# Kernel tuning notes

Hardware: AMD Instinct MI355X
Metric: run time of the kernel (lower is better)

Reference implementation:

```python
import jax, jax.numpy as jnp
import numpy as np

DIM = 2048
KV_DIM = 1024
NUM_HEADS = 16
HEAD_DIM = DIM // NUM_HEADS  # 128
EPS = 1e-6
B, LQ, LKV = 2, 4096, 1024


def _rope_cos_sin(L, d, base=10000.0):
    inv_freq = 1.0 / (base ** (np.arange(0, d, 2, dtype=np.float32) / d))  # [d/2]
    freqs = np.arange(L, dtype=np.float32)[:, None] * inv_freq[None, :]   # [L, d/2]
    emb = np.concatenate([freqs, freqs], axis=-1)                          # [L, d]
    return jnp.asarray(np.cos(emb)), jnp.asarray(np.sin(emb))


def setup_inputs() -> dict:
    key = jax.random.key(0)
    ks = jax.random.split(key, 10)
    x = jax.random.normal(ks[0], (B, LQ, DIM), dtype=jnp.float32)
    y = jax.random.normal(ks[1], (B, LKV, KV_DIM), dtype=jnp.float32)
    xc, xs = _rope_cos_sin(LQ, HEAD_DIM)
    yc, ys = _rope_cos_sin(LKV, HEAD_DIM)
    x_cos = jnp.broadcast_to(xc[None], (B, LQ, HEAD_DIM))
    x_sin = jnp.broadcast_to(xs[None], (B, LQ, HEAD_DIM))
    y_cos = jnp.broadcast_to(yc[None], (B, LKV, HEAD_DIM))
    y_sin = jnp.broadcast_to(ys[None], (B, LKV, HEAD_DIM))
    s = 0.02
    Wq = jax.random.normal(ks[2], (DIM, DIM), dtype=jnp.float32) * s
    Wk = jax.random.normal(ks[3], (DIM, KV_DIM), dtype=jnp.float32) * s
    Wv = jax.random.normal(ks[4], (DIM, KV_DIM), dtype=jnp.float32) * s
    Wo = jax.random.normal(ks[5], (DIM, DIM), dtype=jnp.float32) * s
    bq = jnp.zeros((DIM,), jnp.float32)
    bk = jnp.zeros((DIM,), jnp.float32)
    bv = jnp.zeros((DIM,), jnp.float32)
    bo = jnp.zeros((DIM,), jnp.float32)
    rmsq_w = jnp.ones((DIM,), jnp.float32)
    rmsk_w = jnp.ones((DIM,), jnp.float32)
    ln_w = jnp.ones((KV_DIM,), jnp.float32)
    ln_b = jnp.zeros((KV_DIM,), jnp.float32)
    return dict(x=x, y=y, x_cos=x_cos, x_sin=x_sin, y_cos=y_cos, y_sin=y_sin,
                Wq=Wq, bq=bq, Wk=Wk, bk=bk, Wv=Wv, bv=bv, Wo=Wo, bo=bo,
                rmsq_w=rmsq_w, rmsk_w=rmsk_w, ln_w=ln_w, ln_b=ln_b)


def _rms_norm(t, w, eps=EPS):
    return t * jax.lax.rsqrt(jnp.mean(t * t, axis=-1, keepdims=True) + eps) * w


def _layer_norm(t, w, b, eps=EPS):
    mu = jnp.mean(t, axis=-1, keepdims=True)
    var = jnp.mean(jnp.square(t - mu), axis=-1, keepdims=True)
    return (t - mu) * jax.lax.rsqrt(var + eps) * w + b


def _rotate_half(t):
    d2 = t.shape[-1] // 2
    return jnp.concatenate([-t[..., d2:], t[..., :d2]], axis=-1)


def _apply_rope(t, cos, sin):
    # t: [B, L, H, D]; cos/sin: [B, L, D] -> unsqueeze head dim (unsqueeze_dim=2)
    cos = cos[:, :, None, :]
    sin = sin[:, :, None, :]
    return t * cos + _rotate_half(t) * sin


def _block_forward(x, y, x_cos, x_sin, y_cos, y_sin,
                   Wq, bq, Wk, bk, Wv, bv, Wo, bo,
                   rmsq_w, rmsk_w, ln_w, ln_b):
    Bb, Lq, D = x.shape
    Lk = y.shape[1]
    H, Dh = NUM_HEADS, HEAD_DIM
    # y pre-norm (block-level LayerNorm)
    yn = _layer_norm(y, ln_w, ln_b)
    # projections + RMSNorm on q/k
    q = _rms_norm(x @ Wq.T + bq, rmsq_w)   # [B, Lq, D]
    k = _rms_norm(yn @ Wk.T + bk, rmsk_w)  # [B, Lk, D]
    v = yn @ Wv.T + bv                     # [B, Lk, D]
    # split heads and apply RoPE
    q = _apply_rope(q.reshape(Bb, Lq, H, Dh), x_cos, x_sin)
    k = _apply_rope(k.reshape(Bb, Lk, H, Dh), y_cos, y_sin)
    v = v.reshape(Bb, Lk, H, Dh)
    # non-causal cross attention, scale = 1/sqrt(head_dim)
    scale = 1.0 / jnp.sqrt(jnp.asarray(Dh, q.dtype))
    scores = jnp.einsum('blhd,bmhd->bhlm', q, k) * scale
    probs = jax.nn.softmax(scores, axis=-1)
    out = jnp.einsum('bhlm,bmhd->blhd', probs, v).reshape(Bb, Lq, D)
    return out @ Wo.T + bo


def reference(x, y, x_cos, x_sin, y_cos, y_sin,
              Wq, bq, Wk, bk, Wv, bv, Wo, bo,
              rmsq_w, rmsk_w, ln_w, ln_b):
    return _block_forward(x, y, x_cos, x_sin, y_cos, y_sin,
                          Wq, bq, Wk, bk, Wv, bv, Wo, bo,
                          rmsq_w, rmsk_w, ln_w, ln_b)
```

## Files before the change

kernel.cpp:

```cpp
#include <hip/hip_runtime.h>


typedef __attribute__((ext_vector_type(8))) short    short8;
typedef __attribute__((ext_vector_type(8))) unsigned short ushort8;
typedef __attribute__((ext_vector_type(4))) unsigned short ushort4v;
typedef __attribute__((ext_vector_type(4))) float    f32x4;
typedef __attribute__((ext_vector_type(16))) float   f32x16;
typedef __attribute__((ext_vector_type(4))) unsigned int uint4v;

#define DEV __device__ __forceinline__

DEV unsigned short f2bf(float f) {
  unsigned int u = __builtin_bit_cast(unsigned int, f);
  u += 0x7FFFu + ((u >> 16) & 1u);
  return (unsigned short)(u >> 16);
}
DEV float bf2f(unsigned short h) {
  return __builtin_bit_cast(float, ((unsigned int)h) << 16);
}
DEV unsigned int cvtpk_bf16(float lo, float hi) {
  unsigned int r;
  asm("v_cvt_pk_bf16_f32 %0, %1, %2" : "=v"(r) : "v"(lo), "v"(hi));
  return r;
}
DEV short8 mk8(unsigned a, unsigned b, unsigned c, unsigned d) {
  uint4v t; t.x = a; t.y = b; t.z = c; t.w = d;
  return __builtin_bit_cast(short8, t);
}

DEV void gload_lds16(const void* g, void* l) {
  __builtin_amdgcn_global_load_lds(
      (const __attribute__((address_space(1))) void*)g,
      (__attribute__((address_space(3))) void*)l, 16, 0, 0);
}

__global__ __launch_bounds__(256) void prep_kernel(const float* __restrict__ y,
                                                   const float* __restrict__ lnw,
                                                   const float* __restrict__ lnb,
                                                   unsigned short* __restrict__ yn,
                                                   const float* __restrict__ x,
                                                   const float* __restrict__ Wq,
                                                   const float* __restrict__ Wk,
                                                   const float* __restrict__ Wv,
                                                   const float* __restrict__ Wo,
                                                   unsigned short* __restrict__ xb,
                                                   unsigned short* __restrict__ Wqb,
                                                   unsigned short* __restrict__ Wkb,
                                                   unsigned short* __restrict__ Wvb,
                                                   unsigned short* __restrict__ Wob) {
  const int t = threadIdx.x;
  if (blockIdx.x < 2048) {
    const int row = blockIdx.x;
    const float* yr = y + (size_t)row * 1024;
    float4 v = *(const float4*)(yr + t * 4);
    float s1 = v.x + v.y + v.z + v.w;
    float s2 = v.x * v.x + v.y * v.y + v.z * v.z + v.w * v.w;
#pragma unroll
    for (int m = 1; m < 64; m <<= 1) {
      s1 += __shfl_xor(s1, m);
      s2 += __shfl_xor(s2, m);
    }
    __shared__ float red[8];
    const int wave = t >> 6, lane = t & 63;
    if (lane == 0) { red[wave] = s1; red[4 + wave] = s2; }
    __syncthreads();
    s1 = red[0] + red[1] + red[2] + red[3];
    s2 = red[4] + red[5] + red[6] + red[7];
    const float mu = s1 * (1.0f / 1024.0f);
    const float var = s2 * (1.0f / 1024.0f) - mu * mu;
    const float rs = rsqrtf(var + 1e-6f);
    ushort4v o;
    o.x = f2bf((v.x - mu) * rs * lnw[t * 4 + 0] + lnb[t * 4 + 0]);
    o.y = f2bf((v.y - mu) * rs * lnw[t * 4 + 1] + lnb[t * 4 + 1]);
    o.z = f2bf((v.z - mu) * rs * lnw[t * 4 + 2] + lnb[t * 4 + 2]);
    o.w = f2bf((v.w - mu) * rs * lnw[t * 4 + 3] + lnb[t * 4 + 3]);
    *(ushort4v*)(yn + (size_t)row * 1024 + t * 4) = o;
    return;
  }
  const int nx = 4194304, nwq = 1048576, nwk = 524288, nwv = 524288;
  const int total = 7340032;
  int i = (blockIdx.x - 2048) * 256 + t;
  const int stride = 1536 * 256;
  for (; i < total; i += stride) {
    int j = i;
    const float* s; unsigned short* d;
    if (j < nx) { s = x; d = xb; }
    else if ((j -= nx) < nwq) { s = Wq; d = Wqb; }
    else if ((j -= nwq) < nwk) { s = Wk; d = Wkb; }
    else if ((j -= nwk) < nwv) { s = Wv; d = Wvb; }
    else { j -= nwv; s = Wo; d = Wob; }
    float4 v = *(const float4*)(s + (size_t)j * 4);
    ushort4v o;
    o.x = f2bf(v.x); o.y = f2bf(v.y); o.z = f2bf(v.z); o.w = f2bf(v.w);
    *(ushort4v*)(d + (size_t)j * 4) = o;
  }
}

template <int EPI>
DEV void gemm256_body(const unsigned short* __restrict__ A,
                      const unsigned short* __restrict__ W,
                      const float* __restrict__ bias0,
                      const float* __restrict__ bias1,
                      int nsplit, void* __restrict__ Cout,
                      int M, int N, int K, int ldRow,
                      int bidLocal, int nwg, char* ldsb, int tid) {
  const int wave = tid >> 6, lane = tid & 63;
  const int lg = lane >> 4, l15 = lane & 15;
  const int wm = wave >> 2, wn = wave & 3;

  const int wgid = (bidLocal & 7) * (nwg >> 3) + (bidLocal >> 3);
  const int nbn = N >> 8;
  const int m0 = (wgid / nbn) * 256;
  const int n0 = (wgid % nbn) * 256;

  const char* Ab = (const char*)A;
  const char* Wb = (const char*)W;
  const size_t ld = (size_t)ldRow * 2;
  const int NT = K >> 6;
  const int NI = NT >> 1;

  const int prow = tid >> 3;
  const int psw  = ((tid * 16) & 127) ^ ((prow & 7) << 4);
  const int pdst = tid * 16;
  const char* pAg = Ab + (size_t)(m0 + prow) * ld + psw;
  const char* pBg = Wb + (size_t)(n0 + prow) * ld + psw;

  f32x4 acc[8][4] = {};
  short8 af[4][2];
  short8 bf[4][2];

#define LDSB(BUF, SEG) (ldsb + ((BUF) * 4 + (SEG)) * 16384)

#define STG(BUF, HALF, ISB, TAU) do {                                         \
    const char* _g = ((ISB) ? pBg : pAg) + (size_t)(HALF) * 128 * ld +        \
                     (size_t)(TAU) * 128;                                     \
    char* _l = LDSB(BUF, (ISB) * 2 + (HALF));                                 \
    gload_lds16(_g, _l + pdst);                                               \
    gload_lds16(_g + 64 * ld, _l + pdst + 8192);                              \
  } while (0)

#define LDA(BUF, H) do {                                                      \
    const char* _b = LDSB(BUF, wm);                                           \
    _Pragma("unroll") for (int mfl = 0; mfl < 4; ++mfl) {                     \
      const int _r = (H) * 64 + mfl * 16 + l15;                               \
      _Pragma("unroll") for (int ks = 0; ks < 2; ++ks)                        \
        af[mfl][ks] = *(const short8*)(_b + _r * 128 +                        \
                        ((ks * 64 + lg * 16) ^ ((_r & 7) << 4)));             \
    }                                                                         \
  } while (0)

#define LDB(BUF, G) do {                                                      \
    const char* _b = LDSB(BUF, 2 + (wn >> 1));                                \
    _Pragma("unroll") for (int nfl = 0; nfl < 2; ++nfl) {                     \
      const int _r = (wn & 1) * 64 + (G) * 32 + nfl * 16 + l15;               \
      _Pragma("unroll") for (int ks = 0; ks < 2; ++ks)                        \
        bf[(G) * 2 + nfl][ks] = *(const short8*)(_b + _r * 128 +              \
                        ((ks * 64 + lg * 16) ^ ((_r & 7) << 4)));             \
    }                                                                         \
  } while (0)

#define MFMA_Q(H, G) do {                                                     \
    __builtin_amdgcn_s_setprio(1);                                            \
    _Pragma("unroll") for (int ks = 0; ks < 2; ++ks)                          \
    _Pragma("unroll") for (int mfl = 0; mfl < 4; ++mfl)                       \
    _Pragma("unroll") for (int nfl = 0; nfl < 2; ++nfl)                       \
      acc[(H) * 4 + mfl][(G) * 2 + nfl] =                                     \
        __builtin_amdgcn_mfma_f32_16x16x32_bf16(af[mfl][ks],                  \
            bf[(G) * 2 + nfl][ks], acc[(H) * 4 + mfl][(G) * 2 + nfl], 0,0,0); \
    __builtin_amdgcn_s_setprio(0);                                            \
  } while (0)

#define BAR() __builtin_amdgcn_s_barrier()
#define VM4() asm volatile("s_waitcnt vmcnt(4)" ::: "memory")
#define VM0() asm volatile("s_waitcnt vmcnt(0)" ::: "memory")

  STG(0, 0, 0, 0); STG(0, 1, 0, 0); STG(0, 0, 1, 0); STG(0, 1, 1, 0);
  STG(1, 0, 1, 1); STG(1, 1, 1, 1);
  VM4(); BAR();

  for (int t = 0; t < NI - 1; ++t) {
    const int t2 = 2 * t;
    LDA(0, 0); LDB(0, 0); STG(1, 0, 0, t2 + 1);
    BAR(); MFMA_Q(0, 0); BAR();
    LDB(0, 1); STG(1, 1, 0, t2 + 1);
    BAR(); MFMA_Q(0, 1); BAR();
    LDA(0, 1); STG(0, 0, 1, t2 + 2);
    BAR(); MFMA_Q(1, 1); BAR();
    STG(0, 1, 1, t2 + 2);
    BAR(); MFMA_Q(1, 0); VM4(); BAR();
    LDA(1, 0); LDB(1, 0); STG(0, 0, 0, t2 + 2);
    BAR(); MFMA_Q(0, 0); BAR();
    LDB(1, 1); STG(0, 1, 0, t2 + 2);
    BAR(); MFMA_Q(0, 1); BAR();
    LDA(1, 1); STG(1, 0, 1, t2 + 3);
    BAR(); MFMA_Q(1, 1); BAR();
    STG(1, 1, 1, t2 + 3);
    BAR(); MFMA_Q(1, 0); VM4(); BAR();
  }

  LDA(0, 0); LDB(0, 0); STG(1, 0, 0, NT - 1);
  BAR(); MFMA_Q(0, 0); BAR();
  LDB(0, 1); STG(1, 1, 0, NT - 1);
  BAR(); MFMA_Q(0, 1); BAR();
  LDA(0, 1);
  BAR(); MFMA_Q(1, 1); BAR();
  BAR(); MFMA_Q(1, 0); VM0(); BAR();
  LDA(1, 0); LDB(1, 0); MFMA_Q(0, 0);
  LDB(1, 1); MFMA_Q(0, 1);
  LDA(1, 1); MFMA_Q(1, 1);
  MFMA_Q(1, 0);

#undef STG
#undef LDA
#undef LDB
#undef MFMA_Q
#undef BAR
#undef VM4
#undef VM0
#undef LDSB

#pragma unroll
  for (int nf = 0; nf < 4; ++nf) {
    const int n = n0 + wn * 64 + nf * 16 + l15;
    float bv = 0.f;
    if constexpr (EPI != 2) bv = (n < nsplit) ? bias0[n] : bias1[n - nsplit];
#pragma unroll
    for (int mf = 0; mf < 8; ++mf) {
      const int mB = m0 + wm * 128 + mf * 16 + lg * 4;
#pragma unroll
      for (int r = 0; r < 4; ++r) {
        const float v = acc[mf][nf][r] + bv;
        if constexpr (EPI == 1)
          ((float*)Cout)[(size_t)(mB + r) * N + n] = v;
        else
          ((unsigned short*)Cout)[(size_t)(mB + r) * N + n] = f2bf(v);
      }
    }
  }
}

__global__ __launch_bounds__(512, 2) void gemm_dual(const unsigned short* __restrict__ xb,
                                                    const unsigned short* __restrict__ Wqb,
                                                    const float* __restrict__ bq,
                                                    unsigned short* __restrict__ qpre,
                                                    const unsigned short* __restrict__ ynb,
                                                    const unsigned short* __restrict__ Wkb,
                                                    unsigned short* __restrict__ kvpA,
                                                    unsigned short* __restrict__ kvpB) {
  __shared__ __align__(16) char lds[2][4][16384];
  gemm256_body<0>(xb, Wqb, bq, bq, 2048, qpre, 8192, 2048, 2048, 2048,
                  blockIdx.x, 256, &lds[0][0][0], threadIdx.x);
  __syncthreads();
  const int kvt = blockIdx.x & 127, khalf = blockIdx.x >> 7;
  gemm256_body<2>(ynb + khalf * 512, Wkb + khalf * 512, nullptr, nullptr, 0,
                  khalf ? kvpB : kvpA, 2048, 4096, 512, 1024,
                  kvt, 128, &lds[0][0][0], threadIdx.x);
}

__global__ __launch_bounds__(512, 2) void gemm_f32(const unsigned short* __restrict__ A,
                                                   const unsigned short* __restrict__ W,
                                                   const float* __restrict__ bias,
                                                   float* __restrict__ C,
                                                   int M, int N, int K) {
  __shared__ __align__(16) char lds[2][4][16384];
  gemm256_body<1>(A, W, bias, bias, N, C, M, N, K, K,
                  blockIdx.x, 256, &lds[0][0][0], threadIdx.x);
}

DEV void rmsrope2_body(const unsigned short* __restrict__ in,
                       const unsigned short* __restrict__ in2,
                       const float* __restrict__ bias,
                       const float* __restrict__ w,
                       const float* __restrict__ cs,
                       const float* __restrict__ sn,
                       unsigned short* __restrict__ out,
                       int L, int ldin, float scale, int row,
                       float* srow, float* red) {
  const int t = threadIdx.x;
  ushort8 v = *(const ushort8*)(in + (size_t)row * ldin + t * 8);
  float vals[8];
  if (in2) {
    ushort8 v2 = *(const ushort8*)(in2 + (size_t)row * ldin + t * 8);
#pragma unroll
    for (int j = 0; j < 8; ++j) vals[j] = bf2f(v[j]) + bf2f(v2[j]) + bias[t * 8 + j];
  } else {
#pragma unroll
    for (int j = 0; j < 8; ++j) vals[j] = bf2f(v[j]);
  }
  float ss = 0.f;
#pragma unroll
  for (int j = 0; j < 8; ++j) { ss += vals[j] * vals[j]; srow[t * 8 + j] = vals[j]; }
#pragma unroll
  for (int m = 1; m < 64; m <<= 1) ss += __shfl_xor(ss, m);
  const int wave = t >> 6, lane = t & 63;
  if (lane == 0) red[wave] = ss;
  __syncthreads();
  const float tot = red[0] + red[1] + red[2] + red[3];
  const float rms = rsqrtf(tot * (1.0f / 2048.0f) + 1e-6f);

  const int n0 = t * 8;
  const int d0 = n0 & 127;
  const int hh = n0 >> 7;
  const float sign = (d0 < 64) ? -1.0f : 1.0f;
  const float* cb = cs + (size_t)row * 128 + d0;
  const float* sb = sn + (size_t)row * 128 + d0;
  ushort8 ou;
#pragma unroll
  for (int j = 0; j < 8; ++j) {
    const float self = vals[j] * rms * w[n0 + j];
    const float part = srow[(n0 ^ 64) + j] * rms * w[(n0 ^ 64) + j];
    ou[j] = f2bf((self * cb[j] + sign * part * sb[j]) * scale);
  }
  const int b = row / L, l = row - (row / L) * L;
  *(ushort8*)(out + (((size_t)(b * 16 + hh)) * L + l) * 128 + d0) = ou;
}

DEV void vtrans2_body(const unsigned short* __restrict__ va,
                      const unsigned short* __restrict__ vb,
                      const float* __restrict__ bv,
                      unsigned short* __restrict__ vt, int ldv, int bid,
                      unsigned short (*lt)[130]) {
  const int kt = bid & 15, bh = bid >> 4;
  const int h = bh & 15, b = bh >> 4;
  const int t = threadIdx.x;
  const int i0 = t >> 4, c0 = (t & 15) * 8;
  const size_t sbase = ((size_t)(b * 1024 + kt * 64)) * ldv + h * 128;
#pragma unroll
  for (int ii = 0; ii < 4; ++ii) {
    const int i = i0 + ii * 16;
    ushort8 a = *(const ushort8*)(va + sbase + (size_t)i * ldv + c0);
    ushort8 bb = *(const ushort8*)(vb + sbase + (size_t)i * ldv + c0);
#pragma unroll
    for (int j = 0; j < 8; ++j)
      lt[i][c0 + j] = f2bf(bf2f(a[j]) + bf2f(bb[j]) + bv[h * 128 + c0 + j]);
  }
  __syncthreads();
  const int d0 = t >> 3, j0 = (t & 7) * 8;
  unsigned short* dst = vt + (size_t)bh * 128 * 1024 + kt * 64;
#pragma unroll
  for (int dd = 0; dd < 4; ++dd) {
    const int d = d0 + dd * 32;
    ushort8 o;
#pragma unroll
    for (int jj = 0; jj < 8; ++jj) o[jj] = lt[j0 + jj][d];
    *(ushort8*)(dst + (size_t)d * 1024 + j0) = o;
  }
}

__global__ __launch_bounds__(256) void post_kernel(const unsigned short* __restrict__ qpre,
                                                   const float* __restrict__ rmsq_w,
                                                   const float* __restrict__ x_cos,
                                                   const float* __restrict__ x_sin,
                                                   unsigned short* __restrict__ qr,
                                                   const unsigned short* __restrict__ kvpA,
                                                   const unsigned short* __restrict__ kvpB,
                                                   const float* __restrict__ bk,
                                                   const float* __restrict__ bv,
                                                   const float* __restrict__ rmsk_w,
                                                   const float* __restrict__ y_cos,
                                                   const float* __restrict__ y_sin,
                                                   unsigned short* __restrict__ kr,
                                                   unsigned short* __restrict__ vt,
                                                   float qscale) {
  __shared__ __align__(16) float srow[2048];
  __shared__ float red[4];
  __shared__ unsigned short lt[64][130];
  const int b = blockIdx.x;
  if (b < 8192) {
    rmsrope2_body(qpre, nullptr, nullptr, rmsq_w, x_cos, x_sin, qr,
                  4096, 2048, qscale, b, srow, red);
  } else if (b < 10240) {
    rmsrope2_body(kvpA, kvpB, bk, rmsk_w, y_cos, y_sin, kr,
                  1024, 4096, 1.0f, b - 8192, srow, red);
  } else {
    vtrans2_body(kvpA + 2048, kvpB + 2048, bv, vt, 4096, b - 10240, lt);
  }
}

__global__ __launch_bounds__(256, 2) void attn_kernel(const unsigned short* __restrict__ q,
                                                      const unsigned short* __restrict__ k,
                                                      const unsigned short* __restrict__ vt,
                                                      unsigned short* __restrict__ ao) {
  __shared__ __align__(16) char sK[2][64 * 256];
  __shared__ __align__(16) char sV[2][64 * 256];

  const int bid0 = blockIdx.x;
  const int bid = (bid0 & 7) * 128 + (bid0 >> 3);
  const int qt = bid & 31, bh = bid >> 5;
  const int tid = threadIdx.x;
  const int wave = tid >> 6, lane = tid & 63;
  const int l31 = lane & 31, hi = lane >> 5;
  const bool hib = (hi != 0);

  const unsigned short* qbase = q + (((size_t)bh * 4096) + qt * 128 + wave * 32) * 128;
  const char* kbase = (const char*)(k + (size_t)bh * 1024 * 128);
  const char* vbase = (const char*)(vt + (size_t)bh * 128 * 1024);

  short8 qb[8];
#pragma unroll
  for (int step = 0; step < 8; ++step)
    qb[step] = *(const short8*)(qbase + (size_t)l31 * 128 + step * 16 + hi * 8);

  f32x16 o[4] = {};
  float lsum = 0.f;

#define STAGE_KV(BUF, KV0) do {                                              \
    _Pragma("unroll")                                                        \
    for (int i = 0; i < 4; ++i) {                                            \
      const int p = (i * 256 + tid) * 16;                                    \
      const int row = p >> 8;                                                \
      const int si = (p & 255) ^ ((row & 15) << 4);                          \
      gload_lds16(kbase + (size_t)((KV0) + row) * 256 + si, sK[BUF] + p);    \
    }                                                                        \
    _Pragma("unroll")                                                        \
    for (int i = 0; i < 4; ++i) {                                            \
      const int p = (i * 256 + tid) * 16;                                    \
      const int row = p >> 8;                                                \
      const int si = (p & 255) ^ ((row & 15) << 4);                          \
      const int d = 2 * row + (si >> 7);                                     \
      gload_lds16(vbase + (size_t)d * 2048 + (KV0) * 2 + (si & 127),         \
                  sV[BUF] + p);                                              \
    }                                                                        \
  } while (0)

#define QK(K, S0, S1) do {                                                   \
    const int ksw = (l31 & 15) << 4;                                         \
    _Pragma("unroll") for (int step = 0; step < 8; ++step) {                 \
      const int cb2 = step * 32 + hi * 16;                                   \
      short8 kf0 = *(const short8*)((K) + l31 * 256 + (cb2 ^ ksw));          \
      short8 kf1 = *(const short8*)((K) + (32 + l31) * 256 + (cb2 ^ ksw));   \
      S0 = __builtin_amdgcn_mfma_f32_32x32x16_bf16(kf0, qb[step], S0, 0,0,0);\
      S1 = __builtin_amdgcn_mfma_f32_32x32x16_bf16(kf1, qb[step], S1, 0,0,0);\
    }                                                                        \
  } while (0)

#define SOFTMAX_PV(V, SS, F) do {                                            \
    float p_[16];                                                            \
    _Pragma("unroll") for (int r = 0; r < 16; ++r) p_[r] = exp2f((SS)[r]);   \
    lsum += (((p_[0]+p_[1])+(p_[2]+p_[3])) + ((p_[4]+p_[5])+(p_[6]+p_[7])))  \
          + (((p_[8]+p_[9])+(p_[10]+p_[11])) + ((p_[12]+p_[13])+(p_[14]+p_[15])));\
    const unsigned w0 = cvtpk_bf16(p_[0], p_[1]),  w1 = cvtpk_bf16(p_[2], p_[3]), \
                   w2 = cvtpk_bf16(p_[4], p_[5]),  w3 = cvtpk_bf16(p_[6], p_[7]), \
                   w4 = cvtpk_bf16(p_[8], p_[9]),  w5 = cvtpk_bf16(p_[10], p_[11]),\
                   w6 = cvtpk_bf16(p_[12], p_[13]),w7 = cvtpk_bf16(p_[14], p_[15]);\
    const unsigned x0 = (unsigned)__shfl_xor((int)(hib ? w0 : w2), 32);      \
    const unsigned x1 = (unsigned)__shfl_xor((int)(hib ? w1 : w3), 32);      \
    const unsigned x2 = (unsigned)__shfl_xor((int)(hib ? w4 : w6), 32);      \
    const unsigned x3 = (unsigned)__shfl_xor((int)(hib ? w5 : w7), 32);      \
    const short8 fr0 = mk8(hib ? x0 : w0, hib ? x1 : w1,                     \
                           hib ? w2 : x0, hib ? w3 : x1);                    \
    const short8 fr1 = mk8(hib ? x2 : w4, hib ? x3 : w5,                     \
                           hib ? w6 : x2, hib ? w7 : x3);                    \
    _Pragma("unroll") for (int kstep = 0; kstep < 2; ++kstep) {              \
      const short8 pa = kstep ? fr1 : fr0;                                   \
      const int colb = (F) * 64 + kstep * 32 + hi * 16;                      \
      _Pragma("unroll") for (int dt = 0; dt < 4; ++dt) {                     \
        const int vrow = dt * 16 + (l31 >> 1);                               \
        const int inner = (l31 & 1) * 128 + colb;                            \
        short8 vf = *(const short8*)((V) + vrow * 256 +                      \
                                     (inner ^ ((vrow & 15) << 4)));          \
        o[dt] = __builtin_amdgcn_mfma_f32_32x32x16_bf16(pa, vf, o[dt], 0,0,0);\
      }                                                                      \
    }                                                                        \
  } while (0)

#define TILE(BUF) do {                                                       \
    f32x16 s0 = {}, s1 = {};                                                 \
    QK(sK[BUF], s0, s1);                                                     \
    SOFTMAX_PV(sV[BUF], s0, 0);                                              \
    SOFTMAX_PV(sV[BUF], s1, 1);                                              \
  } while (0)

  STAGE_KV(0, 0);
  __syncthreads();

#pragma unroll 1
  for (int kt2 = 0; kt2 < 8; ++kt2) {
    STAGE_KV(1, (2 * kt2 + 1) * 64);
    TILE(0);
    __syncthreads();
    if (kt2 < 7) STAGE_KV(0, (2 * kt2 + 2) * 64);
    TILE(1);
    __syncthreads();
  }
#undef STAGE_KV
#undef QK
#undef SOFTMAX_PV
#undef TILE

  lsum += __shfl_xor(lsum, 32);
  const float linv = 1.0f / lsum;
  const int b = bh >> 4, h = bh & 15;
#pragma unroll
  for (int r = 0; r < 16; ++r) {
    const int crow = (r & 3) + 8 * (r >> 2) + 4 * hi;
    const float inv = __shfl(linv, crow);
    const int qg = qt * 128 + wave * 32 + crow;
    const size_t orow = ((size_t)b * 4096 + qg) * 2048 + h * 128;
#pragma unroll
    for (int dt = 0; dt < 4; ++dt)
      ao[orow + dt * 32 + l31] = f2bf(o[dt][r] * inv);
  }
}

extern "C" void kernel_launch(void* const* d_in, const int* in_sizes, int n_in,
                              void* d_out, int out_size, void* d_ws, size_t ws_size,
                              hipStream_t stream) {
  (void)in_sizes; (void)n_in; (void)out_size; (void)ws_size;
  const float* x      = (const float*)d_in[0];
  const float* y      = (const float*)d_in[1];
  const float* x_cos  = (const float*)d_in[2];
  const float* x_sin  = (const float*)d_in[3];
  const float* y_cos  = (const float*)d_in[4];
  const float* y_sin  = (const float*)d_in[5];
  const float* Wq     = (const float*)d_in[6];
  const float* bq     = (const float*)d_in[7];
  const float* Wk     = (const float*)d_in[8];
  const float* bk     = (const float*)d_in[9];
  const float* Wv     = (const float*)d_in[10];
  const float* bv     = (const float*)d_in[11];
  const float* Wo     = (const float*)d_in[12];
  const float* bo     = (const float*)d_in[13];
  const float* rmsq_w = (const float*)d_in[14];
  const float* rmsk_w = (const float*)d_in[15];
  const float* ln_w   = (const float*)d_in[16];
  const float* ln_b   = (const float*)d_in[17];

  char* ws = (char*)d_ws;
  unsigned short* xb    = (unsigned short*)(ws + 0);
  unsigned short* Wqb   = (unsigned short*)(ws + 33554432);
  unsigned short* Wkb   = (unsigned short*)(ws + 41943040);
  unsigned short* Wvb   = (unsigned short*)(ws + 46137344);
  unsigned short* Wob   = (unsigned short*)(ws + 50331648);
  unsigned short* ynb   = (unsigned short*)(ws + 58720256);
  unsigned short* qpre  = (unsigned short*)(ws + 62914560);
  unsigned short* kvpA  = (unsigned short*)(ws + 96468992);
  unsigned short* kvpB  = (unsigned short*)(ws + 113246208);
  unsigned short* qr    = xb;
  unsigned short* kr    = Wqb;
  unsigned short* vt    = Wkb;
  unsigned short* ao    = qpre;
  (void)Wvb;

  const float qscale = 1.4426950408889634f * 0.08838834764831843f;

  prep_kernel<<<3584, 256, 0, stream>>>(y, ln_w, ln_b, ynb, x, Wq, Wk, Wv, Wo,
                                        xb, Wqb, Wkb, Wvb, Wob);
  gemm_dual<<<256, 512, 0, stream>>>(xb, Wqb, bq, qpre, ynb, Wkb, kvpA, kvpB);
  post_kernel<<<10752, 256, 0, stream>>>(qpre, rmsq_w, x_cos, x_sin, qr,
                                         kvpA, kvpB, bk, bv, rmsk_w,
                                         y_cos, y_sin, kr, vt, qscale);
  attn_kernel<<<1024, 256, 0, stream>>>(qr, kr, vt, ao);
  gemm_f32<<<256, 512, 0, stream>>>(ao, Wob, bo, (float*)d_out, 8192, 2048, 2048);
}
```

Before: 302.7 us.

## Switch projection GEMM to 32x32x16 bf16 MFMA with paired-row LDS swizzle

Replaces the 16x16x32 MFMA tiling in the shared 256x256 GEMM body with 32x32x16 MFMA. The LDS layout becomes two rows per 256-byte line with a 16-way XOR swizzle, and the fragment loads and epilogue row mapping are rewritten to match. The intent is fewer MFMA instructions and fewer LDS fragment reads per FLOP, since larger MFMA tiles give more operand reuse. The risk is new bank-conflict patterns and a more scattered epilogue store layout.

```diff
diff --git a/kernel.cpp b/kernel.cpp
--- a/kernel.cpp
+++ b/kernel.cpp
@@ -105,7 +105,7 @@
                       int M, int N, int K, int ldRow,
                       int bidLocal, int nwg, char* ldsb, int tid) {
   const int wave = tid >> 6, lane = tid & 63;
-  const int lg = lane >> 4, l15 = lane & 15;
+  const int l31 = lane & 31, hi = lane >> 5;
   const int wm = wave >> 2, wn = wave & 3;
 
   const int wgid = (bidLocal & 7) * (nwg >> 3) + (bidLocal >> 3);
@@ -119,15 +119,15 @@
   const int NT = K >> 6;
   const int NI = NT >> 1;
 
-  const int prow = tid >> 3;
-  const int psw  = ((tid * 16) & 127) ^ ((prow & 7) << 4);
-  const int pdst = tid * 16;
-  const char* pAg = Ab + (size_t)(m0 + prow) * ld + psw;
-  const char* pBg = Wb + (size_t)(n0 + prow) * ld + psw;
-
-  f32x4 acc[8][4] = {};
-  short8 af[4][2];
-  short8 bf[4][2];
+  const int prow2 = tid >> 4;
+  const int psw   = ((tid * 16) & 255) ^ ((prow2 & 15) << 4);
+  const int pdst  = tid * 16;
+  const char* pAg = Ab + (size_t)(m0 + 2 * prow2 + (psw >> 7)) * ld + (psw & 127);
+  const char* pBg = Wb + (size_t)(n0 + 2 * prow2 + (psw >> 7)) * ld + (psw & 127);
+
+  f32x16 acc[4][2] = {};
+  short8 af[2][4];
+  short8 bf[2][4];
 
 #define LDSB(BUF, SEG) (ldsb + ((BUF) * 4 + (SEG)) * 16384)
 
@@ -141,32 +141,33 @@
 
 #define LDA(BUF, H) do {                                                      \
     const char* _b = LDSB(BUF, wm);                                           \
-    _Pragma("unroll") for (int mfl = 0; mfl < 4; ++mfl) {                     \
-      const int _r = (H) * 64 + mfl * 16 + l15;                               \
-      _Pragma("unroll") for (int ks = 0; ks < 2; ++ks)                        \
-        af[mfl][ks] = *(const short8*)(_b + _r * 128 +                        \
-                        ((ks * 64 + lg * 16) ^ ((_r & 7) << 4)));             \
+    _Pragma("unroll") for (int mf = 0; mf < 2; ++mf) {                        \
+      const int ar = (H) * 64 + mf * 32 + l31;                                \
+      const int _r = ar >> 1;                                                 \
+      const int swz = (_r & 15) << 4;                                         \
+      _Pragma("unroll") for (int ks = 0; ks < 4; ++ks)                        \
+        af[mf][ks] = *(const short8*)(_b + _r * 256 +                         \
+                       (((ar & 1) * 128 + ks * 32 + hi * 16) ^ swz));         \
     }                                                                         \
   } while (0)
 
 #define LDB(BUF, G) do {                                                      \
     const char* _b = LDSB(BUF, 2 + (wn >> 1));                                \
-    _Pragma("unroll") for (int nfl = 0; nfl < 2; ++nfl) {                     \
-      const int _r = (wn & 1) * 64 + (G) * 32 + nfl * 16 + l15;               \
-      _Pragma("unroll") for (int ks = 0; ks < 2; ++ks)                        \
-        bf[(G) * 2 + nfl][ks] = *(const short8*)(_b + _r * 128 +              \
-                        ((ks * 64 + lg * 16) ^ ((_r & 7) << 4)));             \
-    }                                                                         \
+    const int br = (wn & 1) * 64 + (G) * 32 + l31;                            \
+    const int _r = br >> 1;                                                   \
+    const int swz = (_r & 15) << 4;                                           \
+    _Pragma("unroll") for (int ks = 0; ks < 4; ++ks)                          \
+      bf[G][ks] = *(const short8*)(_b + _r * 256 +                            \
+                     (((br & 1) * 128 + ks * 32 + hi * 16) ^ swz));           \
   } while (0)
 
 #define MFMA_Q(H, G) do {                                                     \
     __builtin_amdgcn_s_setprio(1);                                            \
-    _Pragma("unroll") for (int ks = 0; ks < 2; ++ks)                          \
-    _Pragma("unroll") for (int mfl = 0; mfl < 4; ++mfl)                       \
-    _Pragma("unroll") for (int nfl = 0; nfl < 2; ++nfl)                       \
-      acc[(H) * 4 + mfl][(G) * 2 + nfl] =                                     \
-        __builtin_amdgcn_mfma_f32_16x16x32_bf16(af[mfl][ks],                  \
-            bf[(G) * 2 + nfl][ks], acc[(H) * 4 + mfl][(G) * 2 + nfl], 0,0,0); \
+    _Pragma("unroll") for (int ks = 0; ks < 4; ++ks)                          \
+    _Pragma("unroll") for (int mf = 0; mf < 2; ++mf)                          \
+      acc[(H) * 2 + mf][G] =                                                  \
+        __builtin_amdgcn_mfma_f32_32x32x16_bf16(af[mf][ks], bf[G][ks],        \
+                                                acc[(H) * 2 + mf][G], 0,0,0); \
     __builtin_amdgcn_s_setprio(0);                                            \
   } while (0)
 
@@ -220,20 +221,21 @@
 #undef LDSB
 
 #pragma unroll
-  for (int nf = 0; nf < 4; ++nf) {
-    const int n = n0 + wn * 64 + nf * 16 + l15;
+  for (int nf = 0; nf < 2; ++nf) {
+    const int n = n0 + wn * 64 + nf * 32 + l31;
     float bv = 0.f;
     if constexpr (EPI != 2) bv = (n < nsplit) ? bias0[n] : bias1[n - nsplit];
 #pragma unroll
-    for (int mf = 0; mf < 8; ++mf) {
-      const int mB = m0 + wm * 128 + mf * 16 + lg * 4;
-#pragma unroll
-      for (int r = 0; r < 4; ++r) {
-        const float v = acc[mf][nf][r] + bv;
+    for (int mfr = 0; mfr < 4; ++mfr) {
+      const int mB = m0 + wm * 128 + mfr * 32 + 4 * hi;
+#pragma unroll
+      for (int r = 0; r < 16; ++r) {
+        const int row = mB + (r & 3) + 8 * (r >> 2);
+        const float v = acc[mfr][nf][r] + bv;
         if constexpr (EPI == 1)
-          ((float*)Cout)[(size_t)(mB + r) * N + n] = v;
+          ((float*)Cout)[(size_t)row * N + n] = v;
         else
-          ((unsigned short*)Cout)[(size_t)(mB + r) * N + n] = f2bf(v);
+          ((unsigned short*)Cout)[(size_t)row * N + n] = f2bf(v);
       }
     }
   }
```

Result: no change. 307.9 us (+1.7%).
